# Performance work log

Measured on AMD Instinct MI355X. Metric: run time of the kernel, lower is better.

The kernel has to match this reference:

```python
import jax, jax.numpy as jnp
import numpy as np

C = 64  # num_channels
B, H, W = 16, 160, 160


def squeeze2d(x, f=2):
    b, c, h, w = x.shape
    x = x.reshape(b, c, h // f, f, w // f, f)
    x = x.transpose(0, 1, 3, 5, 2, 4)
    return x.reshape(b, c * f * f, h // f, w // f)


def unsqueeze2d(x, f=2):
    b, c, h, w = x.shape
    x = x.reshape(b, c // (f * f), f, f, h, w)
    x = x.transpose(0, 1, 4, 2, 5, 3)
    return x.reshape(b, c // (f * f), h * f, w * f)


def get_indices(num_channels):
    # generate_ind(p) tiles the row-major-flattened 2x2 pattern over C//4 channel groups
    def gen(p):
        return np.tile(np.array(p, dtype=bool), num_channels // 4)
    m = np.ones(num_channels, dtype=bool)
    t = gen([0, 0, 1, 1]); b = ~t
    l = gen([0, 1, 0, 1]); r = ~l
    return (m, t, b, l, r, t & l, t & r, b & l, b & r)


INDS = get_indices(C)


def conv1x1(z, w):
    # 1x1 conv == channel matmul
    return jnp.einsum('oc,bchw->bohw', w, z)


def partition_input(x):
    z = unsqueeze2d(x)
    z = jnp.pad(z, ((0, 0), (0, 0), (1, 1), (1, 1)), constant_values=-1.0)
    z = squeeze2d(z)  # (B, C, H+1, W+1)
    m, t, b, l, r, tl, tr, bl, br = INDS
    return (z[:, :, 1:-1, 1:-1],
            z[:, t, :1, 1:-1], z[:, b, -1:, 1:-1],
            z[:, l, 1:-1, :1], z[:, r, 1:-1, -1:],
            z[:, tl, :1, :1], z[:, tr, :1, -1:],
            z[:, bl, -1:, :1], z[:, br, -1:, -1:])


def unsqueeze_line(ze):
    b, c = ze.shape[:2]
    sz = (1, -1) if ze.shape[-2] == 1 else (-1, 1)
    return ze.reshape(b, c // 2, 2, -1).transpose(0, 1, 3, 2).reshape(b, c // 2, *sz)


def merge_output(z_m, z_t, z_b, z_l, z_r, z_tl, z_tr, z_bl, z_br):
    z_m = unsqueeze2d(z_m)
    z_t, z_b, z_l, z_r = [unsqueeze_line(zi) for zi in (z_t, z_b, z_l, z_r)]
    z_tt = jnp.concatenate([z_tl, z_t, z_tr], axis=3)
    z_mm = jnp.concatenate([z_l, z_m, z_r], axis=3)
    z_bb = jnp.concatenate([z_bl, z_b, z_br], axis=3)
    return squeeze2d(jnp.concatenate([z_tt, z_mm, z_bb], axis=2))


def setup_inputs() -> dict:
    key = jax.random.key(0)
    k1, k2 = jax.random.split(key)
    x = jax.random.normal(k1, (B, C, H, W), dtype=jnp.float32)
    logdet = jax.random.normal(k2, (B,), dtype=jnp.float32)
    rng = np.random.RandomState(0)
    w_init = np.linalg.qr(rng.randn(C, C))[0].astype(np.float32)
    weight = jnp.asarray(w_init)
    return {"input": x, "logdet": logdet, "weight": weight}


def reference(input, logdet, weight):
    h, w = input.shape[-2:]
    pixels = [(h - 1) * (w - 1), w - 1, w - 1, h - 1, h - 1, 1, 1, 1, 1]
    ws = [weight[np.ix_(ind, ind)] for ind in INDS]
    dlogdet = sum(jnp.linalg.slogdet(wi)[1] * p for wi, p in zip(ws, pixels))
    zs = partition_input(input)
    outs = [conv1x1(z, wi) for z, wi in zip(zs, ws)]
    output = merge_output(*outs)
    return output, logdet + dlogdet
```

## Files before the change

### kernel.cpp

```cpp
#include <hip/hip_runtime.h>
#include <math.h>

#define NB 16
#define NC 64
#define HW 160
#define PLANE (HW * HW)
#define SG 161
#define SGSQ (SG * SG)
#define NSITES (NB * SGSQ)
#define OUT_LD_OFF (NB * NC * PLANE)
#define TILE 256
#define NCONV ((NSITES + TILE - 1) / TILE)

#define SMEM_FLOATS (32 * 256)

__device__ inline int chmap(int i, int n, int pa, int pb) {
    if (n == 64) return i;
    if (n == 32) return ((i >> 1) << 2) | ((i & 1) ? pb : pa);
    return (i << 2) | pa;
}

__device__ float wave_lu_logabsdet(const float* __restrict__ W, float* A,
                                   int n, int sh, int pa, int pb, int lane) {
    for (int e = lane; e < n * n; e += 64) {
        int i = e >> sh, j = e & (n - 1);
        A[e] = W[chmap(i, n, pa, pb) * 64 + chmap(j, n, pa, pb)];
    }
    asm volatile("s_waitcnt lgkmcnt(0) vmcnt(0)" ::: "memory");
    float logdet = 0.f;
    for (int k = 0; k < n; ++k) {
        float cand = -1.f;
        int idx = k;
        if (lane >= k && lane < n) {
            cand = fabsf(A[(lane << sh) + k]);
            idx = lane;
        }
        for (int off = 32; off; off >>= 1) {
            float oc = __shfl_down(cand, off, 64);
            int oi = __shfl_down(idx, off, 64);
            if (oc > cand) { cand = oc; idx = oi; }
        }
        int p = __shfl(idx, 0, 64);
        if (p != k && lane < n) {
            float tk = A[(k << sh) + lane];
            float tp = A[(p << sh) + lane];
            A[(k << sh) + lane] = tp;
            A[(p << sh) + lane] = tk;
        }
        asm volatile("s_waitcnt lgkmcnt(0)" ::: "memory");
        float piv = A[(k << sh) + k];
        logdet += logf(fabsf(piv));
        float rpiv = 1.f / piv;
        float ckj = (lane < n) ? A[(k << sh) + lane] : 0.f;
        bool act = (lane > k) && (lane < n);
        for (int i2 = k + 1; i2 < n; ++i2) {
            float aik = A[(i2 << sh) + k];
            float mult = aik * rpiv;
            if (act) A[(i2 << sh) + lane] = fmaf(-mult, ckj, A[(i2 << sh) + lane]);
        }
        asm volatile("s_waitcnt lgkmcnt(0)" ::: "memory");
    }
    return logdet;
}

__global__ __launch_bounds__(256, 4) void InvConv1x1GridAlign_kernel(
    const float* __restrict__ x, const float* __restrict__ ld_in,
    const float* __restrict__ W, float* __restrict__ out) {
    __shared__ __align__(16) float smem[SMEM_FLOATS];
    const int tid = threadIdx.x;

    if (blockIdx.x == 0) {
        float* A64 = smem;
        float* A32a = smem + 4096;
        float* A32b = smem + 5120;
        float* A16 = smem + 6144;
        float* partial = smem + 6400;
        int wid = tid >> 6;
        int lane = tid & 63;
        float part = 0.f;
        if (wid == 0) {
            part = 25281.f * wave_lu_logabsdet(W, A64, 64, 6, 0, 0, lane);
        } else if (wid == 1) {
            part  = wave_lu_logabsdet(W, A32a, 32, 5, 2, 3, lane);
            part += wave_lu_logabsdet(W, A32a, 32, 5, 0, 1, lane);
            part *= 159.f;
        } else if (wid == 2) {
            part  = wave_lu_logabsdet(W, A32b, 32, 5, 1, 3, lane);
            part += wave_lu_logabsdet(W, A32b, 32, 5, 0, 2, lane);
            part *= 159.f;
        } else {
            part  = wave_lu_logabsdet(W, A16, 16, 4, 3, 0, lane);
            part += wave_lu_logabsdet(W, A16, 16, 4, 2, 0, lane);
            part += wave_lu_logabsdet(W, A16, 16, 4, 1, 0, lane);
            part += wave_lu_logabsdet(W, A16, 16, 4, 0, 0, lane);
        }
        if (lane == 0) partial[wid] = part;
        __syncthreads();
        if (tid < NB) {
            float dl = partial[0] + partial[1] + partial[2] + partial[3];
            out[OUT_LD_OFF + tid] = ld_in[tid] + dl;
        }
        return;
    }

    const int tile0 = ((int)blockIdx.x - 1) * TILE;
    const int lane = tid & 63;
    const int wid = tid >> 6;
    const int wo = __builtin_amdgcn_readfirstlane(wid << 4);

    float acc[16][4];
#pragma unroll
    for (int j = 0; j < 16; ++j)
#pragma unroll
        for (int s2 = 0; s2 < 4; ++s2) acc[j][s2] = 0.f;

    for (int half = 0; half < 2; ++half) {
        __syncthreads();
        {
            const int scol = (tid & 31) << 3;
#pragma unroll
            for (int p = 0; p < 4; ++p) {
                const int krow = (tid >> 5) + (p << 3);
                const int k = (half << 5) + krow;
                const int pl = k ^ 3;
                const int dy = (k >> 1) & 1, dx = k & 1;
                const int s0 = tile0 + scol;
                unsigned us = (unsigned)s0;
                unsigned b0 = us / SGSQ;
                unsigned rr = us - b0 * SGSQ;
                unsigned Y0 = rr / SG;
                unsigned X0 = rr - Y0 * SG;
                float vals[8];
#pragma unroll
                for (int j = 0; j < 8; ++j) {
                    unsigned X = X0 + j, Y = Y0, b = b0;
                    if (X >= SG) { X -= SG; ++Y; if (Y >= SG) { Y = 0; ++b; } }
                    float vv = 0.f;
                    int py = (int)Y - 1 + dy;
                    int px = (int)X - 1 + dx;
                    if ((s0 + j) < NSITES && (unsigned)py < HW && (unsigned)px < HW)
                        vv = x[(size_t)b * (NC * PLANE) + (size_t)pl * PLANE +
                               (unsigned)(py * HW + px)];
                    vals[j] = vv;
                }
                float* dst = &smem[krow * 256 + scol];
                *(float4*)(dst) = make_float4(vals[0], vals[1], vals[2], vals[3]);
                *(float4*)(dst + 4) = make_float4(vals[4], vals[5], vals[6], vals[7]);
            }
        }
        __syncthreads();
        const float* vrow = smem + (lane << 2);
#pragma unroll 4
        for (int kk = 0; kk < 32; ++kk) {
            const int k = (half << 5) + kk;
            float w[16];
#pragma unroll
            for (int j = 0; j < 16; ++j) w[j] = W[(wo + j) * 64 + k];
            const float4 v4 = *(const float4*)(vrow + (kk << 8));
#pragma unroll
            for (int j = 0; j < 16; ++j) {
                acc[j][0] = fmaf(w[j], v4.x, acc[j][0]);
                acc[j][1] = fmaf(w[j], v4.y, acc[j][1]);
                acc[j][2] = fmaf(w[j], v4.z, acc[j][2]);
                acc[j][3] = fmaf(w[j], v4.w, acc[j][3]);
            }
        }
    }

    const int sbase = tile0 + (lane << 2);
    unsigned Ys[4], Xs[4];
    size_t obase[4];
    bool okv[4];
    {
        unsigned us = (unsigned)sbase;
        unsigned b0 = us / SGSQ;
        unsigned rr = us - b0 * SGSQ;
        unsigned Y0 = rr / SG;
        unsigned X0 = rr - Y0 * SG;
#pragma unroll
        for (int s2 = 0; s2 < 4; ++s2) {
            unsigned X = X0 + s2, Y = Y0, b = b0;
            if (X >= SG) { X -= SG; ++Y; if (Y >= SG) { Y = 0; ++b; } }
            Ys[s2] = Y;
            Xs[s2] = X;
            obase[s2] = (size_t)b * (NC * PLANE);
            okv[s2] = (sbase + s2) < NSITES;
        }
    }
#pragma unroll
    for (int j = 0; j < 16; ++j) {
        const int o = wo + j;
        const int pl = o ^ 3;
        const int dy = (o >> 1) & 1, dx = o & 1;
#pragma unroll
        for (int s2 = 0; s2 < 4; ++s2) {
            int py = (int)Ys[s2] - 1 + dy;
            int px = (int)Xs[s2] - 1 + dx;
            if (okv[s2] && (unsigned)py < HW && (unsigned)px < HW)
                out[obase[s2] + (size_t)pl * PLANE + (unsigned)(py * HW + px)] =
                    acc[j][s2];
        }
    }
}

extern "C" void kernel_launch(void* const* d_in, const int* in_sizes, int n_in,
                              void* d_out, int out_size, void* d_ws, size_t ws_size,
                              hipStream_t stream) {
    const float* x = (const float*)d_in[0];
    const float* ld = (const float*)d_in[1];
    const float* W = (const float*)d_in[2];
    float* out = (float*)d_out;
    hipLaunchKernelGGL(InvConv1x1GridAlign_kernel, dim3(NCONV + 1), dim3(256), 0,
                       stream, x, ld, W, out);
}
```

Baseline: 263.8 us.

## Remap site-to-thread ownership for coalesced loads/stores and vectorized weight reads

Each thread now loads one site per channel, so consecutive threads read consecutive pixels and global loads coalesce. Site and boundary indexing is computed once per thread instead of per element. In the matmul, each lane owns sites strided by 64, which keeps output stores coalesced. Weights are read as float4 over four k values, and activations come from LDS as scalars. The cost is more scalar LDS reads and changed unrolling.

```diff
diff --git a/kernel.cpp b/kernel.cpp
--- a/kernel.cpp
+++ b/kernel.cpp
@@ -108,97 +108,97 @@
     const int wid = tid >> 6;
     const int wo = __builtin_amdgcn_readfirstlane(wid << 4);
 
+    const int offm[4] = {0, 1, HW, HW + 1};
+    bool vm[4];
+    int baseoff;
+    const float* xb;
+    {
+        int s = tile0 + tid;
+        bool sok = s < NSITES;
+        unsigned us = (unsigned)(sok ? s : 0);
+        unsigned b = us / SGSQ;
+        unsigned rr = us - b * SGSQ;
+        unsigned Y = rr / SG;
+        unsigned X = rr - Y * SG;
+        xb = x + (size_t)b * (NC * PLANE);
+        baseoff = ((int)Y - 1) * HW + ((int)X - 1);
+        bool okT = sok && (Y >= 1), okB = sok && (Y <= HW - 1);
+        bool okL = (X >= 1), okR = (X <= HW - 1);
+        vm[0] = okT && okL; vm[1] = okT && okR;
+        vm[2] = okB && okL; vm[3] = okB && okR;
+    }
+
     float acc[16][4];
 #pragma unroll
     for (int j = 0; j < 16; ++j)
 #pragma unroll
         for (int s2 = 0; s2 < 4; ++s2) acc[j][s2] = 0.f;
 
+#pragma unroll 1
     for (int half = 0; half < 2; ++half) {
         __syncthreads();
-        {
-            const int scol = (tid & 31) << 3;
-#pragma unroll
-            for (int p = 0; p < 4; ++p) {
-                const int krow = (tid >> 5) + (p << 3);
-                const int k = (half << 5) + krow;
-                const int pl = k ^ 3;
-                const int dy = (k >> 1) & 1, dx = k & 1;
-                const int s0 = tile0 + scol;
-                unsigned us = (unsigned)s0;
-                unsigned b0 = us / SGSQ;
-                unsigned rr = us - b0 * SGSQ;
-                unsigned Y0 = rr / SG;
-                unsigned X0 = rr - Y0 * SG;
-                float vals[8];
+#pragma unroll 8
+        for (int krow = 0; krow < 32; ++krow) {
+            const int k = (half << 5) + krow;
+            const int pl = k ^ 3;
+            const int m = krow & 3;
+            float val = vm[m] ? xb[pl * PLANE + baseoff + offm[m]] : 0.f;
+            smem[(krow << 8) + tid] = val;
+        }
+        __syncthreads();
+#pragma unroll 1
+        for (int kb = 0; kb < 8; ++kb) {
+            float v[4][4];
+            const float* vb = smem + (kb << 10) + lane;
+#pragma unroll
+            for (int kk = 0; kk < 4; ++kk)
+#pragma unroll
+                for (int s2 = 0; s2 < 4; ++s2)
+                    v[kk][s2] = vb[(kk << 8) + (s2 << 6)];
+            const int k0 = (half << 5) + (kb << 2);
+#pragma unroll
+            for (int jb = 0; jb < 2; ++jb) {
+                float4 w4[8];
+#pragma unroll
+                for (int j = 0; j < 8; ++j)
+                    w4[j] = *(const float4*)(W + (wo + (jb << 3) + j) * 64 + k0);
 #pragma unroll
                 for (int j = 0; j < 8; ++j) {
-                    unsigned X = X0 + j, Y = Y0, b = b0;
-                    if (X >= SG) { X -= SG; ++Y; if (Y >= SG) { Y = 0; ++b; } }
-                    float vv = 0.f;
-                    int py = (int)Y - 1 + dy;
-                    int px = (int)X - 1 + dx;
-                    if ((s0 + j) < NSITES && (unsigned)py < HW && (unsigned)px < HW)
-                        vv = x[(size_t)b * (NC * PLANE) + (size_t)pl * PLANE +
-                               (unsigned)(py * HW + px)];
-                    vals[j] = vv;
+                    const int jj = (jb << 3) + j;
+#pragma unroll
+                    for (int kk = 0; kk < 4; ++kk) {
+                        const float wjk = (kk == 0) ? w4[j].x
+                                        : (kk == 1) ? w4[j].y
+                                        : (kk == 2) ? w4[j].z : w4[j].w;
+#pragma unroll
+                        for (int s2 = 0; s2 < 4; ++s2)
+                            acc[jj][s2] = fmaf(wjk, v[kk][s2], acc[jj][s2]);
+                    }
                 }
-                float* dst = &smem[krow * 256 + scol];
-                *(float4*)(dst) = make_float4(vals[0], vals[1], vals[2], vals[3]);
-                *(float4*)(dst + 4) = make_float4(vals[4], vals[5], vals[6], vals[7]);
             }
         }
-        __syncthreads();
-        const float* vrow = smem + (lane << 2);
-#pragma unroll 4
-        for (int kk = 0; kk < 32; ++kk) {
-            const int k = (half << 5) + kk;
-            float w[16];
-#pragma unroll
-            for (int j = 0; j < 16; ++j) w[j] = W[(wo + j) * 64 + k];
-            const float4 v4 = *(const float4*)(vrow + (kk << 8));
-#pragma unroll
-            for (int j = 0; j < 16; ++j) {
-                acc[j][0] = fmaf(w[j], v4.x, acc[j][0]);
-                acc[j][1] = fmaf(w[j], v4.y, acc[j][1]);
-                acc[j][2] = fmaf(w[j], v4.z, acc[j][2]);
-                acc[j][3] = fmaf(w[j], v4.w, acc[j][3]);
-            }
-        }
-    }
-
-    const int sbase = tile0 + (lane << 2);
-    unsigned Ys[4], Xs[4];
-    size_t obase[4];
-    bool okv[4];
-    {
-        unsigned us = (unsigned)sbase;
-        unsigned b0 = us / SGSQ;
-        unsigned rr = us - b0 * SGSQ;
-        unsigned Y0 = rr / SG;
-        unsigned X0 = rr - Y0 * SG;
-#pragma unroll
-        for (int s2 = 0; s2 < 4; ++s2) {
-            unsigned X = X0 + s2, Y = Y0, b = b0;
-            if (X >= SG) { X -= SG; ++Y; if (Y >= SG) { Y = 0; ++b; } }
-            Ys[s2] = Y;
-            Xs[s2] = X;
-            obase[s2] = (size_t)b * (NC * PLANE);
-            okv[s2] = (sbase + s2) < NSITES;
-        }
-    }
-#pragma unroll
-    for (int j = 0; j < 16; ++j) {
-        const int o = wo + j;
-        const int pl = o ^ 3;
-        const int dy = (o >> 1) & 1, dx = o & 1;
-#pragma unroll
-        for (int s2 = 0; s2 < 4; ++s2) {
-            int py = (int)Ys[s2] - 1 + dy;
-            int px = (int)Xs[s2] - 1 + dx;
-            if (okv[s2] && (unsigned)py < HW && (unsigned)px < HW)
-                out[obase[s2] + (size_t)pl * PLANE + (unsigned)(py * HW + px)] =
-                    acc[j][s2];
+    }
+
+#pragma unroll
+    for (int s2 = 0; s2 < 4; ++s2) {
+        int s = tile0 + lane + (s2 << 6);
+        bool sok = s < NSITES;
+        unsigned us = (unsigned)(sok ? s : 0);
+        unsigned b = us / SGSQ;
+        unsigned rr = us - b * SGSQ;
+        unsigned Y = rr / SG;
+        unsigned X = rr - Y * SG;
+        float* ob = out + (size_t)b * (NC * PLANE);
+        int boff = ((int)Y - 1) * HW + ((int)X - 1);
+        bool okT = sok && (Y >= 1), okB = sok && (Y <= HW - 1);
+        bool okL = (X >= 1), okR = (X <= HW - 1);
+        bool wm[4] = {okT && okL, okT && okR, okB && okL, okB && okR};
+#pragma unroll
+        for (int j = 0; j < 16; ++j) {
+            const int o = wo + j;
+            const int pl = o ^ 3;
+            const int m = j & 3;
+            if (wm[m]) ob[pl * PLANE + boff + offm[m]] = acc[j][s2];
         }
     }
 }
```

Result: no change. 262.5 us (-0.5%).
